# Performance work log

Measured on AMD Instinct MI355X. Metric: run time of the kernel, lower is better.

## Reference

```python
import jax, jax.numpy as jnp
import numpy as np
import math

IN_FEATURES = 4096
OUT_FEATURES = 4096
P = max(IN_FEATURES, OUT_FEATURES)   # total_permutations
D = min(IN_FEATURES, OUT_FEATURES)   # diag_length
SPARSITY = 0.1
K = math.ceil(int((1.0 - SPARSITY) * IN_FEATURES * OUT_FEATURES) / D)  # 3687
ALPHA_LR = 0.01
NUM_ITER = 50


def sparse_soft_topk_mask_dykstra(alpha, k, l, num_iter):
    """Dykstra projection of alpha/l onto {0<=m<=1, sum(m)=k} (soft top-k mask)."""
    s = alpha / l
    n = s.shape[0]
    p0 = jnp.zeros_like(s)
    q0 = jnp.zeros_like(s)

    def body(carry, _):
        x, p, q = carry
        # project x+p onto hyperplane sum = k
        t = x + p
        y = t + (k - jnp.sum(t)) / n
        p = t - y
        # project y+q onto box [0, 1]
        u = y + q
        x_new = jnp.clip(u, 0.0, 1.0)
        q = u - x_new
        return (x_new, p, q), None

    (x, _, _), _ = jax.lax.scan(body, (s, p0, q0), None, length=num_iter)
    return x  # last projection is onto the box -> exact zeros / ones


def compute_weight(V, alpha):
    a = sparse_soft_topk_mask_dykstra(alpha, K, ALPHA_LR, NUM_ITER)  # (P,)
    vals = a[:, None] * V                                             # (P, D)
    i = jnp.arange(P)[:, None]
    j = jnp.arange(D)[None, :]
    if OUT_FEATURES >= IN_FEATURES:
        # pseudo-diagonal i: rows shifted by i, column j scaled by V[i, j]
        rows = (i + j) % OUT_FEATURES
        cols = jnp.broadcast_to(j, (P, D))
    else:
        # row r scaled by V[i, r], columns shifted by i
        rows = jnp.broadcast_to(j, (P, D))
        cols = (i + j) % IN_FEATURES
    W = jnp.zeros((OUT_FEATURES, IN_FEATURES), V.dtype)
    W = W.at[rows.reshape(-1), cols.reshape(-1)].add(vals.reshape(-1))
    return W


def setup_inputs() -> dict:
    key = jax.random.key(0)
    k1, k2 = jax.random.split(key)
    # kaiming_uniform_(a=sqrt(5)) over fan_in = D -> bound = sqrt(1/D)
    bound = 1.0 / np.sqrt(D)
    V = jax.random.uniform(k1, (P, D), jnp.float32, -bound, bound)
    alpha = jnp.ones((P,), jnp.float32) / IN_FEATURES
    x = jax.random.normal(k2, (512, IN_FEATURES), jnp.float32)
    return {"x": x, "V": V, "alpha": alpha}


def reference(x, V, alpha):
    W = compute_weight(V, alpha)  # (out, in)
    return x @ W.T                # F.linear(x, W)
```

## Files before the change

kernel.cpp:

```cpp
#include <hip/hip_runtime.h>
#include <hip/hip_bf16.h>
#include <stdint.h>

#define PDIM 4096
#define KSEL 3687.0f
#define NITER 50

typedef unsigned short ushort_t;
typedef __attribute__((ext_vector_type(8))) __bf16 bf16x8;
typedef __attribute__((ext_vector_type(4))) float f32x4;

typedef __attribute__((address_space(3))) void lds_void;
typedef __attribute__((address_space(1))) const void glob_void;

__device__ __forceinline__ ushort_t f32_to_bf16_rne(float f) {
  union { float f; uint32_t u; } v; v.f = f;
  uint32_t r = 0x7FFFu + ((v.u >> 16) & 1u);
  return (ushort_t)((v.u + r) >> 16);
}

__device__ __forceinline__ float bf16_to_f32(ushort_t h) {
  union { uint32_t u; float f; } v; v.u = ((uint32_t)h) << 16;
  return v.f;
}

__device__ __forceinline__ void async_cp16(const void* g, void* l) {
  __builtin_amdgcn_global_load_lds((glob_void*)g, (lds_void*)l, 16, 0, 0);
}

__device__ __forceinline__ void raw_barrier() {
  __builtin_amdgcn_sched_barrier(0);
  asm volatile("" ::: "memory");
  __builtin_amdgcn_s_barrier();
  asm volatile("" ::: "memory");
  __builtin_amdgcn_sched_barrier(0);
}

__device__ __forceinline__ float wave_sum_dpp(float x) {
  float s = x;
  int t;
  t = __builtin_amdgcn_update_dpp(0, __float_as_int(s), 0x111, 0xF, 0xF, true);
  s += __int_as_float(t);
  t = __builtin_amdgcn_update_dpp(0, __float_as_int(s), 0x112, 0xF, 0xF, true);
  s += __int_as_float(t);
  t = __builtin_amdgcn_update_dpp(0, __float_as_int(s), 0x114, 0xF, 0xF, true);
  s += __int_as_float(t);
  t = __builtin_amdgcn_update_dpp(0, __float_as_int(s), 0x118, 0xF, 0xF, true);
  s += __int_as_float(t);
  t = __builtin_amdgcn_update_dpp(0, __float_as_int(s), 0x142, 0xA, 0xF, true);
  s += __int_as_float(t);
  t = __builtin_amdgcn_update_dpp(0, __float_as_int(s), 0x143, 0xC, 0xF, true);
  s += __int_as_float(t);
  return s;
}

__global__ __launch_bounds__(256) void prep_kernel(
    const float* __restrict__ alpha, float* __restrict__ a_out,
    const float* __restrict__ x, ushort_t* __restrict__ Xb, int n4,
    const float* __restrict__ V) {
  if (blockIdx.x >= 1 && blockIdx.x <= 2048) {
    const float4* V4 = (const float4*)V;
    const int base = (blockIdx.x - 1) * 2048 + (int)threadIdx.x;
#pragma unroll
    for (int i = 0; i < 8; ++i) {
      const float4 vv = V4[base + i * 256];
      asm volatile("" :: "v"(vv.x), "v"(vv.y), "v"(vv.z), "v"(vv.w));
    }
    return;
  }
  if (blockIdx.x != 0) {
    const int i = (blockIdx.x - 2049) * 256 + threadIdx.x;
    if (i < n4) {
      const float4 v = ((const float4*)x)[i];
      ushort4 o;
      o.x = f32_to_bf16_rne(v.x);
      o.y = f32_to_bf16_rne(v.y);
      o.z = f32_to_bf16_rne(v.z);
      o.w = f32_to_bf16_rne(v.w);
      ((ushort4*)Xb)[i] = o;
    }
    return;
  }
  __shared__ float red[8];
  const int tid = threadIdx.x;
  const int lane = tid & 63;
  const int wv = tid >> 6;
  float xx[16], q[16];
  float p = 0.0f;
#pragma unroll
  for (int i = 0; i < 16; ++i) {
    xx[i] = alpha[i * 256 + tid] * 100.0f;
    q[i] = 0.0f;
  }
  for (int it = 0; it < NITER; ++it) {
    float t[16];
    float loc = 0.0f;
#pragma unroll
    for (int i = 0; i < 16; ++i) { t[i] = xx[i] + p; loc += t[i]; }
    loc = wave_sum_dpp(loc);
    const int slot = (it & 1) * 4;
    if (lane == 63) red[slot + wv] = loc;
    __syncthreads();
    const float tot = red[slot] + red[slot + 1] + red[slot + 2] + red[slot + 3];
    const float corr = (KSEL - tot) * (1.0f / 4096.0f);
    p = -corr;
#pragma unroll
    for (int i = 0; i < 16; ++i) {
      const float y = t[i] + corr;
      const float u = y + q[i];
      const float xn = fminf(fmaxf(u, 0.0f), 1.0f);
      q[i] = u - xn;
      xx[i] = xn;
    }
  }
#pragma unroll
  for (int i = 0; i < 16; ++i) a_out[i * 256 + tid] = xx[i];
}

__global__ __launch_bounds__(256) void wmat_kernel(
    const float* __restrict__ V, const float* __restrict__ a,
    ushort_t* __restrict__ Wb) {
  __shared__ float vt[192][67];
  const int t = threadIdx.x;
  const int r0 = blockIdx.x * 128;
  const int c0 = blockIdx.y * 64;
  const int dbase = (r0 - c0 - 63 + 2 * PDIM) & (PDIM - 1);
  const int csub = (t & 15) * 4;
  const int rsub = t >> 4;
#pragma unroll
  for (int i = 0; i < 12; ++i) {
    const int ld = i * 16 + rsub;
    const int d = (dbase + ld) & (PDIM - 1);
    const float av = a[d];
    const float4 vv = *(const float4*)(V + (size_t)d * PDIM + c0 + csub);
    vt[ld][csub + 0] = av * vv.x;
    vt[ld][csub + 1] = av * vv.y;
    vt[ld][csub + 2] = av * vv.z;
    vt[ld][csub + 3] = av * vv.w;
  }
  __syncthreads();
#pragma unroll
  for (int k = 0; k < 4; ++k) {
    const int ry = (t >> 3) + k * 32;
    const int cb = (t & 7) * 8;
    ushort_t pk[8];
#pragma unroll
    for (int j = 0; j < 8; ++j) {
      const int c = cb + j;
      pk[j] = f32_to_bf16_rne(vt[ry - c + 63][c]);
    }
    *(uint4*)(Wb + (size_t)(r0 + ry) * PDIM + c0 + cb) = *(const uint4*)pk;
  }
}

__global__ __launch_bounds__(256, 2) void gemm_kernel(
    const ushort_t* __restrict__ Xb, const ushort_t* __restrict__ Wb,
    ushort_t* __restrict__ par) {
  constexpr int Kdim = 4096, KQ = 1024, NIT = KQ / 64;
  __shared__ __align__(16) ushort_t As[2][128 * 64];
  __shared__ __align__(16) ushort_t Bs[2][128 * 64];
  const int tid = threadIdx.x;
  const int lane = tid & 63;
  const int w = tid >> 6;
  const int l15 = lane & 15;
  const int quad = lane >> 4;
  const int bid = blockIdx.x;
  const int u = ((bid & 7) << 6) | (bid >> 3);
  const int z = u & 3;
  const int mblk = (u >> 2) & 3;
  const int nblk = u >> 4;
  const int m0 = mblk * 128;
  const int n0 = nblk * 128;
  const int kbase = z * KQ;
  const int arow = lane >> 3;
  const int aslot = lane & 7;

  f32x4 acc[8][2];
#pragma unroll
  for (int mt = 0; mt < 8; ++mt)
#pragma unroll
    for (int nt = 0; nt < 2; ++nt) acc[mt][nt] = (f32x4){0.f, 0.f, 0.f, 0.f};

  auto stage = [&](int buf, int it) {
    const int k0 = kbase + it * 64;
#pragma unroll
    for (int s = w; s < 16; s += 4) {
      const int row = s * 8 + arow;
      const int j = aslot ^ (row & 7);
      async_cp16(Xb + (size_t)(m0 + row) * Kdim + k0 + j * 8,
                 (char*)&As[buf][0] + (size_t)s * 1024);
      async_cp16(Wb + (size_t)(n0 + row) * Kdim + k0 + j * 8,
                 (char*)&Bs[buf][0] + (size_t)s * 1024);
    }
  };

  stage(0, 0);
  for (int it = 0; it < NIT; ++it) {
    const int cur = it & 1;
    if (it < NIT - 1) {
      stage(cur ^ 1, it + 1);
      asm volatile("s_waitcnt vmcnt(8)" ::: "memory");
    } else {
      asm volatile("s_waitcnt vmcnt(0)" ::: "memory");
    }
    raw_barrier();
    const ushort_t* __restrict__ Ab = &As[cur][0];
    const ushort_t* __restrict__ Bb = &Bs[cur][0];
#pragma unroll
    for (int kk = 0; kk < 64; kk += 32) {
      const int cj = (kk >> 3) + quad;
      bf16x8 bfv[2];
#pragma unroll
      for (int nt = 0; nt < 2; ++nt) {
        const int row = w * 32 + nt * 16 + l15;
        bfv[nt] = *(const bf16x8*)&Bb[(row * 8 + (cj ^ (row & 7))) * 8];
      }
#pragma unroll
      for (int mt = 0; mt < 8; ++mt) {
        const int row = mt * 16 + l15;
        const bf16x8 af = *(const bf16x8*)&Ab[(row * 8 + (cj ^ (row & 7))) * 8];
        acc[mt][0] = __builtin_amdgcn_mfma_f32_16x16x32_bf16(af, bfv[0],
                                                             acc[mt][0], 0, 0, 0);
        acc[mt][1] = __builtin_amdgcn_mfma_f32_16x16x32_bf16(af, bfv[1],
                                                             acc[mt][1], 0, 0, 0);
      }
    }
    raw_barrier();
  }
  const int tile = nblk * 4 + mblk;
  ushort_t* pbase = par + ((size_t)z * 128 + tile) * 16384;
#pragma unroll
  for (int mt = 0; mt < 8; ++mt) {
#pragma unroll
    for (int nt = 0; nt < 2; ++nt) {
      const int slot = mt * 2 + nt;
      ushort4 o;
      o.x = f32_to_bf16_rne(acc[mt][nt][0]);
      o.y = f32_to_bf16_rne(acc[mt][nt][1]);
      o.z = f32_to_bf16_rne(acc[mt][nt][2]);
      o.w = f32_to_bf16_rne(acc[mt][nt][3]);
      *(ushort4*)(pbase + (size_t)(slot * 256 + tid) * 4) = o;
    }
  }
}

__global__ __launch_bounds__(256) void combine_kernel(
    const ushort_t* __restrict__ par, float* __restrict__ out) {
  const int tile = blockIdx.x >> 2;
  const int qh = blockIdx.x & 3;
  const int nblk = tile >> 2;
  const int mblk = tile & 3;
  const int m0 = mblk * 128;
  const int n0 = nblk * 128;
  const int tid = threadIdx.x;
  const int lane = tid & 63;
  const int w = tid >> 6;
  const int l15 = lane & 15;
  const int quad = lane >> 4;
#pragma unroll
  for (int ss = 0; ss < 4; ++ss) {
    const int slot = qh * 4 + ss;
    float s0 = 0.f, s1 = 0.f, s2 = 0.f, s3 = 0.f;
#pragma unroll
    for (int z = 0; z < 4; ++z) {
      const ushort4 v = *(const ushort4*)(par +
          ((size_t)z * 128 + tile) * 16384 + (size_t)(slot * 256 + tid) * 4);
      s0 += bf16_to_f32(v.x);
      s1 += bf16_to_f32(v.y);
      s2 += bf16_to_f32(v.z);
      s3 += bf16_to_f32(v.w);
    }
    const int mt = slot >> 1;
    const int nt = slot & 1;
    const int mb = m0 + mt * 16 + quad * 4;
    const int n = n0 + w * 32 + nt * 16 + l15;
    out[(size_t)(mb + 0) * PDIM + n] = s0;
    out[(size_t)(mb + 1) * PDIM + n] = s1;
    out[(size_t)(mb + 2) * PDIM + n] = s2;
    out[(size_t)(mb + 3) * PDIM + n] = s3;
  }
}

extern "C" void kernel_launch(void* const* d_in, const int* in_sizes, int n_in,
                              void* d_out, int out_size, void* d_ws,
                              size_t ws_size, hipStream_t stream) {
  const float* x = (const float*)d_in[0];
  const float* V = (const float*)d_in[1];
  const float* alpha = (const float*)d_in[2];
  float* out = (float*)d_out;
  const int M = in_sizes[0] / PDIM;

  float* a_mask = (float*)d_ws;
  ushort_t* Xb = (ushort_t*)((char*)d_ws + 16 * 1024);
  ushort_t* Wb = Xb + (size_t)M * PDIM;
  ushort_t* par = Wb + (size_t)PDIM * PDIM;

  const int n4x = (M * PDIM) / 4;
  prep_kernel<<<1 + 2048 + (n4x + 255) / 256, 256, 0, stream>>>(
      alpha, a_mask, x, Xb, n4x, V);
  wmat_kernel<<<dim3(PDIM / 128, PDIM / 64), 256, 0, stream>>>(V, a_mask, Wb);
  gemm_kernel<<<512, 256, 0, stream>>>(Xb, Wb, par);
  combine_kernel<<<512, 256, 0, stream>>>(par, out);
}
```

Baseline: 149.9 us.

## Enlarge GEMM tiles to 256x256 with 8 waves and 8-way split-K

The GEMM moves from 128x128 tiles with 4 waves and 4-way split-K (512 blocks) to 256x256 tiles with 8 waves in a 2x4 layout and 8-way split-K (256 blocks). Each wave computes a 128x64 sub-tile, and B fragments are reused across A fragments in registers, which raises arithmetic intensity and cuts global and LDS traffic per FLOP. The combine kernel now sums 8 bf16 partials per output. In exchange, LDS use doubles to 128KB per block, accumulator register pressure rises, and there are more partial writes and reads plus only 256 blocks to occupy the CUs.

```diff
diff --git a/kernel.cpp b/kernel.cpp
--- a/kernel.cpp
+++ b/kernel.cpp
@@ -153,44 +153,47 @@
   }
 }
 
-__global__ __launch_bounds__(256, 2) void gemm_kernel(
+__global__ __launch_bounds__(512, 2) void gemm_kernel(
     const ushort_t* __restrict__ Xb, const ushort_t* __restrict__ Wb,
     ushort_t* __restrict__ par) {
-  constexpr int Kdim = 4096, KQ = 1024, NIT = KQ / 64;
-  __shared__ __align__(16) ushort_t As[2][128 * 64];
-  __shared__ __align__(16) ushort_t Bs[2][128 * 64];
+  constexpr int Kdim = 4096, KQ = 512, NIT = KQ / 64;
+  __shared__ __align__(16) ushort_t As[2][256 * 64];
+  __shared__ __align__(16) ushort_t Bs[2][256 * 64];
   const int tid = threadIdx.x;
   const int lane = tid & 63;
   const int w = tid >> 6;
   const int l15 = lane & 15;
   const int quad = lane >> 4;
+  const int wr = w >> 2;
+  const int wc = w & 3;
   const int bid = blockIdx.x;
-  const int u = ((bid & 7) << 6) | (bid >> 3);
-  const int z = u & 3;
-  const int mblk = (u >> 2) & 3;
-  const int nblk = u >> 4;
-  const int m0 = mblk * 128;
-  const int n0 = nblk * 128;
+  const int z = bid & 7;
+  const int tile = bid >> 3;
+  const int mblk = tile & 1;
+  const int nblk = tile >> 1;
+  const int m0 = mblk * 256;
+  const int n0 = nblk * 256;
   const int kbase = z * KQ;
-  const int arow = lane >> 3;
-  const int aslot = lane & 7;
-
-  f32x4 acc[8][2];
+  const int crow8 = lane >> 3;
+  const int slotj = lane & 7;
+
+  f32x4 acc[8][4];
 #pragma unroll
   for (int mt = 0; mt < 8; ++mt)
 #pragma unroll
-    for (int nt = 0; nt < 2; ++nt) acc[mt][nt] = (f32x4){0.f, 0.f, 0.f, 0.f};
+    for (int nt = 0; nt < 4; ++nt) acc[mt][nt] = (f32x4){0.f, 0.f, 0.f, 0.f};
 
   auto stage = [&](int buf, int it) {
     const int k0 = kbase + it * 64;
 #pragma unroll
-    for (int s = w; s < 16; s += 4) {
-      const int row = s * 8 + arow;
-      const int j = aslot ^ (row & 7);
+    for (int i = 0; i < 4; ++i) {
+      const int chunk = w * 4 + i;
+      const int row = chunk * 8 + crow8;
+      const int j = slotj ^ (row & 7);
       async_cp16(Xb + (size_t)(m0 + row) * Kdim + k0 + j * 8,
-                 (char*)&As[buf][0] + (size_t)s * 1024);
+                 (char*)&As[buf][0] + (size_t)chunk * 1024);
       async_cp16(Wb + (size_t)(n0 + row) * Kdim + k0 + j * 8,
-                 (char*)&Bs[buf][0] + (size_t)s * 1024);
+                 (char*)&Bs[buf][0] + (size_t)chunk * 1024);
     }
   };
 
@@ -206,74 +209,86 @@
     raw_barrier();
     const ushort_t* __restrict__ Ab = &As[cur][0];
     const ushort_t* __restrict__ Bb = &Bs[cur][0];
-#pragma unroll
-    for (int kk = 0; kk < 64; kk += 32) {
-      const int cj = (kk >> 3) + quad;
-      bf16x8 bfv[2];
-#pragma unroll
-      for (int nt = 0; nt < 2; ++nt) {
-        const int row = w * 32 + nt * 16 + l15;
-        bfv[nt] = *(const bf16x8*)&Bb[(row * 8 + (cj ^ (row & 7))) * 8];
+    bf16x8 bfr[4][2];
+#pragma unroll
+    for (int nt = 0; nt < 4; ++nt)
+#pragma unroll
+      for (int k2 = 0; k2 < 2; ++k2) {
+        const int row = wc * 64 + nt * 16 + l15;
+        const int cj = k2 * 4 + quad;
+        bfr[nt][k2] = *(const bf16x8*)&Bb[(row * 8 + (cj ^ (row & 7))) * 8];
       }
 #pragma unroll
-      for (int mt = 0; mt < 8; ++mt) {
-        const int row = mt * 16 + l15;
-        const bf16x8 af = *(const bf16x8*)&Ab[(row * 8 + (cj ^ (row & 7))) * 8];
-        acc[mt][0] = __builtin_amdgcn_mfma_f32_16x16x32_bf16(af, bfv[0],
-                                                             acc[mt][0], 0, 0, 0);
-        acc[mt][1] = __builtin_amdgcn_mfma_f32_16x16x32_bf16(af, bfv[1],
-                                                             acc[mt][1], 0, 0, 0);
-      }
+    for (int mh = 0; mh < 2; ++mh) {
+      bf16x8 afr[4][2];
+#pragma unroll
+      for (int mi = 0; mi < 4; ++mi)
+#pragma unroll
+        for (int k2 = 0; k2 < 2; ++k2) {
+          const int row = wr * 128 + (mh * 4 + mi) * 16 + l15;
+          const int cj = k2 * 4 + quad;
+          afr[mi][k2] = *(const bf16x8*)&Ab[(row * 8 + (cj ^ (row & 7))) * 8];
+        }
+#pragma unroll
+      for (int mi = 0; mi < 4; ++mi)
+#pragma unroll
+        for (int nt = 0; nt < 4; ++nt) {
+          acc[mh * 4 + mi][nt] = __builtin_amdgcn_mfma_f32_16x16x32_bf16(
+              afr[mi][0], bfr[nt][0], acc[mh * 4 + mi][nt], 0, 0, 0);
+          acc[mh * 4 + mi][nt] = __builtin_amdgcn_mfma_f32_16x16x32_bf16(
+              afr[mi][1], bfr[nt][1], acc[mh * 4 + mi][nt], 0, 0, 0);
+        }
     }
     raw_barrier();
   }
-  const int tile = nblk * 4 + mblk;
-  ushort_t* pbase = par + ((size_t)z * 128 + tile) * 16384;
+  ushort_t* pbase = par + ((size_t)z * 32 + tile) * 65536;
 #pragma unroll
   for (int mt = 0; mt < 8; ++mt) {
 #pragma unroll
-    for (int nt = 0; nt < 2; ++nt) {
-      const int slot = mt * 2 + nt;
+    for (int nt = 0; nt < 4; ++nt) {
+      const int slot = mt * 4 + nt;
       ushort4 o;
       o.x = f32_to_bf16_rne(acc[mt][nt][0]);
       o.y = f32_to_bf16_rne(acc[mt][nt][1]);
       o.z = f32_to_bf16_rne(acc[mt][nt][2]);
       o.w = f32_to_bf16_rne(acc[mt][nt][3]);
-      *(ushort4*)(pbase + (size_t)(slot * 256 + tid) * 4) = o;
-    }
-  }
-}
-
-__global__ __launch_bounds__(256) void combine_kernel(
+      *(ushort4*)(pbase + (size_t)(slot * 512 + tid) * 4) = o;
+    }
+  }
+}
+
+__global__ __launch_bounds__(512) void combine_kernel(
     const ushort_t* __restrict__ par, float* __restrict__ out) {
   const int tile = blockIdx.x >> 2;
   const int qh = blockIdx.x & 3;
-  const int nblk = tile >> 2;
-  const int mblk = tile & 3;
-  const int m0 = mblk * 128;
-  const int n0 = nblk * 128;
+  const int mblk = tile & 1;
+  const int nblk = tile >> 1;
+  const int m0 = mblk * 256;
+  const int n0 = nblk * 256;
   const int tid = threadIdx.x;
   const int lane = tid & 63;
   const int w = tid >> 6;
+  const int wr = w >> 2;
+  const int wc = w & 3;
   const int l15 = lane & 15;
   const int quad = lane >> 4;
 #pragma unroll
-  for (int ss = 0; ss < 4; ++ss) {
-    const int slot = qh * 4 + ss;
+  for (int ss = 0; ss < 8; ++ss) {
+    const int slot = qh * 8 + ss;
     float s0 = 0.f, s1 = 0.f, s2 = 0.f, s3 = 0.f;
 #pragma unroll
-    for (int z = 0; z < 4; ++z) {
+    for (int z = 0; z < 8; ++z) {
       const ushort4 v = *(const ushort4*)(par +
-          ((size_t)z * 128 + tile) * 16384 + (size_t)(slot * 256 + tid) * 4);
+          ((size_t)z * 32 + tile) * 65536 + (size_t)(slot * 512 + tid) * 4);
       s0 += bf16_to_f32(v.x);
       s1 += bf16_to_f32(v.y);
       s2 += bf16_to_f32(v.z);
       s3 += bf16_to_f32(v.w);
     }
-    const int mt = slot >> 1;
-    const int nt = slot & 1;
-    const int mb = m0 + mt * 16 + quad * 4;
-    const int n = n0 + w * 32 + nt * 16 + l15;
+    const int mt = slot >> 2;
+    const int nt = slot & 3;
+    const int mb = m0 + wr * 128 + mt * 16 + quad * 4;
+    const int n = n0 + wc * 64 + nt * 16 + l15;
     out[(size_t)(mb + 0) * PDIM + n] = s0;
     out[(size_t)(mb + 1) * PDIM + n] = s1;
     out[(size_t)(mb + 2) * PDIM + n] = s2;
@@ -299,6 +314,6 @@
   prep_kernel<<<1 + 2048 + (n4x + 255) / 256, 256, 0, stream>>>(
       alpha, a_mask, x, Xb, n4x, V);
   wmat_kernel<<<dim3(PDIM / 128, PDIM / 64), 256, 0, stream>>>(V, a_mask, Wb);
-  gemm_kernel<<<512, 256, 0, stream>>>(Xb, Wb, par);
-  combine_kernel<<<512, 256, 0, stream>>>(par, out);
-}
+  gemm_kernel<<<256, 512, 0, stream>>>(Xb, Wb, par);
+  combine_kernel<<<128, 512, 0, stream>>>(par, out);
+}
```

Result: no change. 152.7 us (+1.9%).
